# Performance work log

Hardware: AMD Instinct MI355X
Metric: run time of the kernel (lower is better)

Reference implementation:

```python
import jax, jax.numpy as jnp
import numpy as np

ALPHA = 3.0   # self.alpha
TAU = 0.1     # contrastive temperature
K = 8         # configs.k (top-k hyperedges per node)


def _scale(x, w, ehy, enod):
    """One scale of incidence_matrix_learn.
    x: [B, L, D] series tokens; w: [ws, D] word tokens;
    ehy: [H, D] hyperedge embedding table; enod: [N, D] node embedding table, N = L + ws.
    Returns (binary incidence matrix [N, H] float32, scalar contrastive loss).
    """
    B = x.shape[0]
    # concat_all[i]: cat(x.permute(0,2,1), word_expanded) -> [B, D, N]
    we = jnp.broadcast_to(w.T[None], (B,) + w.T.shape)          # [B, D, ws]
    concat = jnp.concatenate([jnp.transpose(x, (0, 2, 1)), we], axis=-1)  # [B, D, N]
    N, H = enod.shape[0], ehy.shape[0]
    # adjacency: softmax(relu(alpha * nodeec @ hyperen.T)) along hyperedge dim
    a = enod @ ehy.T                                            # [N, H]
    adj = jax.nn.softmax(jax.nn.relu(ALPHA * a), axis=-1)
    # top-k mask + threshold > 0.5 -> binary incidence matrix
    k = min(H, K)
    _, idx = jax.lax.top_k(adj, k)                              # [N, k]
    mask = jnp.zeros_like(adj).at[jnp.arange(N)[:, None], idx].set(1.0)
    adj_bin = ((adj * mask) > 0.5).astype(jnp.float32)          # [N, H]
    # positives: nodes sharing any hyperedge (build_pos_indices_from_edge_index),
    # equivalent to (A A^T > 0) with self excluded; dropping all-zero columns is a no-op here
    P = (adj_bin @ adj_bin.T > 0) & ~jnp.eye(N, dtype=bool)     # [N, N]
    cnt = P.sum(axis=1)                                         # positives per node
    # acl_loss_batched, vectorized over batch and nodes
    nodes = jnp.transpose(concat, (0, 2, 1))                    # [B, N, D]
    nrm = nodes / jnp.maximum(jnp.linalg.norm(nodes, axis=-1, keepdims=True), 1e-12)
    sim = jnp.einsum('bnd,bmd->bnm', nrm, nrm) / TAU            # [B, N, N]
    denom = jax.nn.logsumexp(sim, axis=-1)                      # [B, N]
    pos_mean = jnp.einsum('bnm,nm->bn', sim, P.astype(sim.dtype)) / jnp.maximum(cnt, 1)
    valid = cnt > 0                                             # [N]
    loss_sum = jnp.sum(jnp.where(valid[None, :], denom - pos_mean, 0.0))
    vc = B * valid.sum()
    loss = jnp.where(vc > 0, loss_sum / jnp.maximum(vc, 1), 0.0)
    return adj_bin, loss


def setup_inputs() -> dict:
    key = jax.random.key(0)
    ks = jax.random.split(key, 8)
    B, D = 64, 512
    return dict(
        x0=jax.random.normal(ks[0], (B, 512, D), dtype=jnp.float32),
        x1=jax.random.normal(ks[1], (B, 256, D), dtype=jnp.float32),
        word0=jax.random.normal(ks[2], (128, D), dtype=jnp.float32),
        word1=jax.random.normal(ks[3], (128, D), dtype=jnp.float32),
        embhy0=jax.random.normal(ks[4], (128, D), dtype=jnp.float32),
        embhy1=jax.random.normal(ks[5], (64, D), dtype=jnp.float32),
        embnod0=jax.random.normal(ks[6], (640, D), dtype=jnp.float32),
        embnod1=jax.random.normal(ks[7], (384, D), dtype=jnp.float32),
    )


def reference(x0, x1, word0, word1, embhy0, embhy1, embnod0, embnod1):
    a0, l0 = _scale(x0, word0, embhy0, embnod0)
    a1, l1 = _scale(x1, word1, embhy1, embnod1)
    return (a0, a1, l0 + l1)
```

## Files before the change

### kernel.cpp

```cpp
#include <hip/hip_runtime.h>


#define DDIM 512
#define BATCH 64
#define NGID 65536
#define NSLOT 5

typedef __attribute__((ext_vector_type(8))) short short8;
typedef __attribute__((ext_vector_type(4))) float f32x4;

__constant__ int PAIR_SCALE[21] = {0,0,0,0,0,0,0,0,0,0,0,0,0,0,0, 1,1,1,1,1,1};
__constant__ int PAIR_TU[21]    = {0,0,0,0,0,1,1,1,1,2,2,2,3,3,4, 0,0,0,1,1,2};
__constant__ int PAIR_TV[21]    = {0,1,2,3,4,1,2,3,4,2,3,4,3,4,4, 0,1,2,1,2,2};

__device__ __forceinline__ unsigned short f2bf(float f) {
  unsigned int u = __float_as_uint(f);
  u += 0x7fffu + ((u >> 16) & 1u);
  return (unsigned short)(u >> 16);
}

__device__ __forceinline__ void async16(const void* g, void* l) {
  __builtin_amdgcn_global_load_lds(
      (const __attribute__((address_space(1))) unsigned int*)g,
      (__attribute__((address_space(3))) unsigned int*)l, 16, 0, 0);
}

__global__ __launch_bounds__(256) void prep_kernel(
    const float* __restrict__ enod0, const float* __restrict__ ehy0,
    const float* __restrict__ enod1, const float* __restrict__ ehy1,
    float* __restrict__ adj0, float* __restrict__ adj1,
    int* __restrict__ labels0, int* __restrict__ labels1,
    const float* __restrict__ x0, const float* __restrict__ w0,
    const float* __restrict__ x1, const float* __restrict__ w1,
    unsigned short* __restrict__ nhat0, unsigned short* __restrict__ nhat1,
    float* __restrict__ acc, int* __restrict__ ticket) {
  const int t = threadIdx.x;
  if (blockIdx.x < 1024) {
    if (blockIdx.x == 0 && t == 0) { acc[0] = 0.f; acc[1] = 0.f; ticket[0] = 0; }
    const bool s0 = blockIdx.x < 640;
    const int n = s0 ? blockIdx.x : blockIdx.x - 640;
    const int H = s0 ? 128 : 64;
    const float* enod = s0 ? enod0 : enod1;
    const float* ehy = s0 ? ehy0 : ehy1;
    float* out_adj = s0 ? adj0 : adj1;
    int* labels = s0 ? labels0 : labels1;
    __shared__ float erow[DDIM];
    __shared__ float red[128];
    __shared__ int lab;
    if (t < 128) ((float4*)erow)[t] = ((const float4*)(enod + (size_t)n * DDIM))[t];
    if (t == 0) lab = -1;
    __syncthreads();
    float v = 0.f;
    if (t < H) {
      const float4* hr = (const float4*)(ehy + (size_t)t * DDIM);
      float a = 0.f;
      #pragma unroll 8
      for (int d = 0; d < DDIM / 4; ++d) {
        float4 h = hr[d];
        float4 e = ((const float4*)erow)[d];
        a = fmaf(h.x, e.x, a); a = fmaf(h.y, e.y, a);
        a = fmaf(h.z, e.z, a); a = fmaf(h.w, e.w, a);
      }
      v = fmaxf(0.f, 3.0f * a);
    }
    if (t < 128) red[t] = v;
    __syncthreads();
    for (int s = 64; s > 0; s >>= 1) {
      if (t < s) red[t] = fmaxf(red[t], red[t + s]);
      __syncthreads();
    }
    const float mx = red[0];
    __syncthreads();
    const float e = (t < H) ? __expf(v - mx) : 0.f;
    if (t < 128) red[t] = e;
    __syncthreads();
    for (int s = 64; s > 0; s >>= 1) {
      if (t < s) red[t] += red[t + s];
      __syncthreads();
    }
    const float sum = red[0];
    if (t < H) {
      const float adj = e / sum;
      const float bin = (adj > 0.5f) ? 1.0f : 0.0f;
      out_adj[(size_t)n * H + t] = bin;
      if (bin > 0.f) lab = t;
    }
    __syncthreads();
    if (t == 0) labels[n] = lab;
  } else {
    const int wave = t >> 6;
    const int lane = t & 63;
    const int g = (blockIdx.x - 1024) * 4 + wave;
    const bool s0 = g < BATCH * 640;
    const int gg = s0 ? g : g - BATCH * 640;
    const int N = s0 ? 640 : 384;
    const int L = s0 ? 512 : 256;
    const float* x = s0 ? x0 : x1;
    const float* w = s0 ? w0 : w1;
    unsigned short* nhat = s0 ? nhat0 : nhat1;
    const int b = gg / N;
    const int n = gg - b * N;
    const float* src = (n < L) ? (x + ((size_t)b * L + n) * DDIM)
                               : (w + (size_t)(n - L) * DDIM);
    const float4* rowp = (const float4*)src;
    const float4 v0 = rowp[lane];
    const float4 v1 = rowp[lane + 64];
    float ss = v0.x * v0.x + v0.y * v0.y + v0.z * v0.z + v0.w * v0.w +
               v1.x * v1.x + v1.y * v1.y + v1.z * v1.z + v1.w * v1.w;
    #pragma unroll
    for (int off = 32; off > 0; off >>= 1) ss += __shfl_xor(ss, off);
    const float rinv = 1.0f / fmaxf(sqrtf(ss), 1e-12f);
    ushort4 o0, o1;
    o0.x = f2bf(v0.x * rinv); o0.y = f2bf(v0.y * rinv);
    o0.z = f2bf(v0.z * rinv); o0.w = f2bf(v0.w * rinv);
    o1.x = f2bf(v1.x * rinv); o1.y = f2bf(v1.y * rinv);
    o1.z = f2bf(v1.z * rinv); o1.w = f2bf(v1.w * rinv);
    ushort4* op = (ushort4*)(nhat + ((size_t)b * N + n) * DDIM);
    op[lane] = o0;
    op[lane + 64] = o1;
  }
}

__global__ __launch_bounds__(256) void cnt_kernel(
    const int* __restrict__ labels0, int* __restrict__ cnt0,
    const int* __restrict__ labels1, int* __restrict__ cnt1,
    int* __restrict__ valid) {
  const bool s0 = blockIdx.x == 0;
  const int* labels = s0 ? labels0 : labels1;
  int* cnt = s0 ? cnt0 : cnt1;
  int* validcnt = s0 ? valid : valid + 1;
  const int N = s0 ? 640 : 384;
  __shared__ int lab[640];
  __shared__ int hist[128];
  __shared__ int vc;
  const int t = threadIdx.x;
  if (t == 0) vc = 0;
  if (t < 128) hist[t] = 0;
  for (int i = t; i < N; i += 256) lab[i] = labels[i];
  __syncthreads();
  for (int i = t; i < N; i += 256)
    if (lab[i] >= 0) atomicAdd(&hist[lab[i]], 1);
  __syncthreads();
  int lv = 0;
  for (int i = t; i < N; i += 256) {
    const int c = (lab[i] >= 0) ? hist[lab[i]] - 1 : 0;
    cnt[i] = c;
    if (c > 0) ++lv;
  }
  if (lv > 0) atomicAdd(&vc, lv);
  __syncthreads();
  if (t == 0) *validcnt = vc;
}

__global__ __launch_bounds__(256) void lse_kernel(
    const unsigned short* __restrict__ nhat0, const int* __restrict__ labels0,
    const unsigned short* __restrict__ nhat1, const int* __restrict__ labels1,
    float2* __restrict__ sp) {
  __shared__ short8 Abuf[2][1024];
  __shared__ short8 Bbuf[2][1024];
  __shared__ int labU[128], labV[128];
  __shared__ float2 rowBuf[128][2];
  __shared__ float2 colBuf[128][2];

  const int tid = threadIdx.x;
  const int p = blockIdx.x >> 6;
  const int b = blockIdx.x & 63;
  const bool s0 = PAIR_SCALE[p] == 0;
  const int tu = PAIR_TU[p], tv = PAIR_TV[p];
  const bool diag = (tu == tv);
  const int N = s0 ? 640 : 384;
  const unsigned short* nhat = s0 ? nhat0 : nhat1;
  const int* labels = s0 ? labels0 : labels1;
  const int gbase = s0 ? b * 640 : 40960 + b * 384;
  const size_t base = (size_t)b * N * DDIM;

  const int w = tid >> 6, lane = tid & 63;
  const int wr = w >> 1, wc = w & 1;
  const int lrow = lane & 15, lq = lane >> 4;

  if (tid < 128) labU[tid] = labels[tu * 128 + tid];
  else labV[tid - 128] = labels[tv * 128 + (tid - 128)];

  const unsigned short* Asrc = nhat + base + (size_t)tu * 128 * DDIM;
  const unsigned short* Bsrc = nhat + base + (size_t)tv * 128 * DDIM;

  #define STAGE(buf, kk)                                                     \
    do {                                                                     \
      _Pragma("unroll")                                                      \
      for (int i = 0; i < 4; ++i) {                                          \
        const int f = i * 4 + w;                                             \
        const int rg = f >> 1, ks = f & 1;                                   \
        const size_t so = (size_t)(rg * 16 + lrow) * DDIM +                  \
                          (kk) * 64 + ks * 32 + lq * 8;                      \
        async16(Asrc + so, &Abuf[buf][f * 64]);                              \
        async16(Bsrc + so, &Bbuf[buf][f * 64]);                              \
      }                                                                      \
    } while (0)

  f32x4 acc[4][4];
  #pragma unroll
  for (int mi = 0; mi < 4; ++mi)
    #pragma unroll
    for (int ni = 0; ni < 4; ++ni) acc[mi][ni] = (f32x4){0.f, 0.f, 0.f, 0.f};

  STAGE(0, 0);
  __syncthreads();

  for (int k = 0; k < 8; ++k) {
    const int cur = k & 1;
    if (k < 7) STAGE(cur ^ 1, k + 1);
    #pragma unroll
    for (int ks = 0; ks < 2; ++ks) {
      short8 am[4], bn[4];
      #pragma unroll
      for (int mi = 0; mi < 4; ++mi)
        am[mi] = Abuf[cur][((wr * 4 + mi) * 2 + ks) * 64 + lane];
      #pragma unroll
      for (int ni = 0; ni < 4; ++ni)
        bn[ni] = Bbuf[cur][((wc * 4 + ni) * 2 + ks) * 64 + lane];
      #pragma unroll
      for (int mi = 0; mi < 4; ++mi)
        #pragma unroll
        for (int ni = 0; ni < 4; ++ni)
          acc[mi][ni] = __builtin_amdgcn_mfma_f32_16x16x32_bf16(
              am[mi], bn[ni], acc[mi][ni], 0, 0, 0);
    }
    __syncthreads();
  }
  #undef STAGE

  float rSE[4][4], rPOS[4][4];
  float cSE[4] = {0.f, 0.f, 0.f, 0.f};
  float cPOS[4] = {0.f, 0.f, 0.f, 0.f};
  int labn[4][4], labm[4];
  #pragma unroll
  for (int mi = 0; mi < 4; ++mi)
    #pragma unroll
    for (int r = 0; r < 4; ++r) {
      rSE[mi][r] = 0.f; rPOS[mi][r] = 0.f;
      labn[mi][r] = labU[wr * 64 + mi * 16 + lq * 4 + r];
    }
  #pragma unroll
  for (int ni = 0; ni < 4; ++ni) labm[ni] = labV[wc * 64 + ni * 16 + lrow];

  #pragma unroll
  for (int mi = 0; mi < 4; ++mi) {
    const int u_loc = wr * 64 + mi * 16 + lq * 4;
    #pragma unroll
    for (int ni = 0; ni < 4; ++ni) {
      const int v_loc = wc * 64 + ni * 16 + lrow;
      #pragma unroll
      for (int r = 0; r < 4; ++r) {
        const float sim = acc[mi][ni][r] * 10.0f;
        const float e = __expf(sim - 10.0f);
        rSE[mi][r] += e;
        const bool match = (labn[mi][r] >= 0) && (labm[ni] == labn[mi][r]);
        const bool self = diag && (u_loc + r == v_loc);
        if (match && !self) rPOS[mi][r] += sim;
        if (!diag) {
          cSE[ni] += e;
          if (match) cPOS[ni] += sim;
        }
      }
    }
  }

  #pragma unroll
  for (int off = 1; off <= 8; off <<= 1)
    #pragma unroll
    for (int mi = 0; mi < 4; ++mi)
      #pragma unroll
      for (int r = 0; r < 4; ++r) {
        rSE[mi][r] += __shfl_xor(rSE[mi][r], off);
        rPOS[mi][r] += __shfl_xor(rPOS[mi][r], off);
      }
  if (lrow == 0) {
    #pragma unroll
    for (int mi = 0; mi < 4; ++mi)
      #pragma unroll
      for (int r = 0; r < 4; ++r) {
        float2 st; st.x = rSE[mi][r]; st.y = rPOS[mi][r];
        rowBuf[wr * 64 + mi * 16 + lq * 4 + r][wc] = st;
      }
  }
  if (!diag) {
    #pragma unroll
    for (int off = 16; off <= 32; off <<= 1)
      #pragma unroll
      for (int ni = 0; ni < 4; ++ni) {
        cSE[ni] += __shfl_xor(cSE[ni], off);
        cPOS[ni] += __shfl_xor(cPOS[ni], off);
      }
    if (lane < 16) {
      #pragma unroll
      for (int ni = 0; ni < 4; ++ni) {
        float2 st; st.x = cSE[ni]; st.y = cPOS[ni];
        colBuf[wc * 64 + ni * 16 + lrow][wr] = st;
      }
    }
  }
  __syncthreads();
  if (tid < 128) {
    const float2 ra = rowBuf[tid][0], rb = rowBuf[tid][1];
    float2 st; st.x = ra.x + rb.x; st.y = ra.y + rb.y;
    sp[(size_t)tv * NGID + gbase + tu * 128 + tid] = st;
    if (!diag) {
      const float2 ca = colBuf[tid][0], cb = colBuf[tid][1];
      float2 ct; ct.x = ca.x + cb.x; ct.y = ca.y + cb.y;
      sp[(size_t)tu * NGID + gbase + tv * 128 + tid] = ct;
    }
  }
}

__global__ __launch_bounds__(256) void loss_reduce(
    const float2* __restrict__ sp, const int* __restrict__ cnt0,
    const int* __restrict__ cnt1, float* __restrict__ acc,
    const int* __restrict__ valid, int* __restrict__ ticket,
    float* __restrict__ lossp) {
  __shared__ float r0[4], r1[4];
  const int t = threadIdx.x;
  float l0 = 0.f, l1 = 0.f;
  for (int g = blockIdx.x * 256 + t; g < NGID; g += 64 * 256) {
    const bool is0 = g < 40960;
    const int n = is0 ? (g % 640) : ((g - 40960) % 384);
    const int nslots = is0 ? 5 : 3;
    float se = 0.f, pos = 0.f;
    for (int s = 0; s < nslots; ++s) {
      const float2 v = sp[(size_t)s * NGID + g];
      se += v.x; pos += v.y;
    }
    const int c = is0 ? cnt0[n] : cnt1[n];
    if (c > 0) {
      const float v = (10.0f + logf(se)) - pos / (float)c;
      if (is0) l0 += v; else l1 += v;
    }
  }
  #pragma unroll
  for (int off = 32; off > 0; off >>= 1) {
    l0 += __shfl_xor(l0, off);
    l1 += __shfl_xor(l1, off);
  }
  if ((t & 63) == 0) { r0[t >> 6] = l0; r1[t >> 6] = l1; }
  __syncthreads();
  if (t == 0) {
    atomicAdd(&acc[0], r0[0] + r0[1] + r0[2] + r0[3]);
    atomicAdd(&acc[1], r1[0] + r1[1] + r1[2] + r1[3]);
    __threadfence();
    const int done = atomicAdd(ticket, 1);
    if (done == 63) {
      const float a0v = atomicAdd(&acc[0], 0.0f);
      const float a1v = atomicAdd(&acc[1], 0.0f);
      float l = 0.f;
      if (valid[0] > 0) l += a0v / (float)(BATCH * valid[0]);
      if (valid[1] > 0) l += a1v / (float)(BATCH * valid[1]);
      lossp[0] = l;
    }
  }
}

extern "C" void kernel_launch(void* const* d_in, const int* in_sizes, int n_in,
                              void* d_out, int out_size, void* d_ws,
                              size_t ws_size, hipStream_t stream) {
  const float* x0 = (const float*)d_in[0];
  const float* x1 = (const float*)d_in[1];
  const float* w0 = (const float*)d_in[2];
  const float* w1 = (const float*)d_in[3];
  const float* ehy0 = (const float*)d_in[4];
  const float* ehy1 = (const float*)d_in[5];
  const float* enod0 = (const float*)d_in[6];
  const float* enod1 = (const float*)d_in[7];

  float* out = (float*)d_out;
  float* adj0 = out;
  float* adj1 = out + 640 * 128;
  float* lossp = out + 640 * 128 + 384 * 64;

  unsigned short* nhat0 = (unsigned short*)d_ws;
  unsigned short* nhat1 = nhat0 + (size_t)BATCH * 640 * DDIM;
  int* ip = (int*)(nhat1 + (size_t)BATCH * 384 * DDIM);
  int* labels0 = ip;
  int* labels1 = labels0 + 640;
  int* cnt0 = labels1 + 384;
  int* cnt1 = cnt0 + 640;
  int* valid = cnt1 + 384;
  int* ticket = valid + 2;
  float* acc = (float*)(ticket + 1);
  float2* sp = (float2*)((((size_t)(acc + 2)) + 255) & ~(size_t)255);

  prep_kernel<<<1024 + 16384, 256, 0, stream>>>(
      enod0, ehy0, enod1, ehy1, adj0, adj1, labels0, labels1,
      x0, w0, x1, w1, nhat0, nhat1, acc, ticket);
  cnt_kernel<<<2, 256, 0, stream>>>(labels0, cnt0, labels1, cnt1, valid);
  lse_kernel<<<1344, 256, 0, stream>>>(nhat0, labels0, nhat1, labels1, sp);
  loss_reduce<<<64, 256, 0, stream>>>(sp, cnt0, cnt1, acc, valid, ticket,
                                      lossp);
}
```

Before: 235.0 us.

## Triple-buffer lse_kernel K loop and fold count kernel into loss reduction

The lse_kernel main loop moves from a double-buffered 64-wide K step with full __syncthreads to a 32-wide step with three LDS slots. It uses explicit vmcnt waits and a raw s_barrier, which keeps two async loads in flight while the MFMAs run. The separate cnt_kernel launch is removed, and every loss_reduce block now recomputes the label histograms and valid counts in shared memory. This saves one kernel launch and the dependency between kernels, at the cost of repeating the histogram work in all 64 reduce blocks and running more barriers per K in the GEMM.

```diff
diff --git a/kernel.cpp b/kernel.cpp
--- a/kernel.cpp
+++ b/kernel.cpp
@@ -4,7 +4,6 @@
 #define DDIM 512
 #define BATCH 64
 #define NGID 65536
-#define NSLOT 5
 
 typedef __attribute__((ext_vector_type(8))) short short8;
 typedef __attribute__((ext_vector_type(4))) float f32x4;
@@ -121,43 +120,12 @@
   }
 }
 
-__global__ __launch_bounds__(256) void cnt_kernel(
-    const int* __restrict__ labels0, int* __restrict__ cnt0,
-    const int* __restrict__ labels1, int* __restrict__ cnt1,
-    int* __restrict__ valid) {
-  const bool s0 = blockIdx.x == 0;
-  const int* labels = s0 ? labels0 : labels1;
-  int* cnt = s0 ? cnt0 : cnt1;
-  int* validcnt = s0 ? valid : valid + 1;
-  const int N = s0 ? 640 : 384;
-  __shared__ int lab[640];
-  __shared__ int hist[128];
-  __shared__ int vc;
-  const int t = threadIdx.x;
-  if (t == 0) vc = 0;
-  if (t < 128) hist[t] = 0;
-  for (int i = t; i < N; i += 256) lab[i] = labels[i];
-  __syncthreads();
-  for (int i = t; i < N; i += 256)
-    if (lab[i] >= 0) atomicAdd(&hist[lab[i]], 1);
-  __syncthreads();
-  int lv = 0;
-  for (int i = t; i < N; i += 256) {
-    const int c = (lab[i] >= 0) ? hist[lab[i]] - 1 : 0;
-    cnt[i] = c;
-    if (c > 0) ++lv;
-  }
-  if (lv > 0) atomicAdd(&vc, lv);
-  __syncthreads();
-  if (t == 0) *validcnt = vc;
-}
-
 __global__ __launch_bounds__(256) void lse_kernel(
     const unsigned short* __restrict__ nhat0, const int* __restrict__ labels0,
     const unsigned short* __restrict__ nhat1, const int* __restrict__ labels1,
     float2* __restrict__ sp) {
-  __shared__ short8 Abuf[2][1024];
-  __shared__ short8 Bbuf[2][1024];
+  __shared__ short8 Abuf[3][512];
+  __shared__ short8 Bbuf[3][512];
   __shared__ int labU[128], labV[128];
   __shared__ float2 rowBuf[128][2];
   __shared__ float2 colBuf[128][2];
@@ -184,16 +152,14 @@
   const unsigned short* Asrc = nhat + base + (size_t)tu * 128 * DDIM;
   const unsigned short* Bsrc = nhat + base + (size_t)tv * 128 * DDIM;
 
-  #define STAGE(buf, kk)                                                     \
+  #define STAGE(slot, cc)                                                    \
     do {                                                                     \
       _Pragma("unroll")                                                      \
-      for (int i = 0; i < 4; ++i) {                                          \
-        const int f = i * 4 + w;                                             \
-        const int rg = f >> 1, ks = f & 1;                                   \
-        const size_t so = (size_t)(rg * 16 + lrow) * DDIM +                  \
-                          (kk) * 64 + ks * 32 + lq * 8;                      \
-        async16(Asrc + so, &Abuf[buf][f * 64]);                              \
-        async16(Bsrc + so, &Bbuf[buf][f * 64]);                              \
+      for (int i = 0; i < 2; ++i) {                                          \
+        const int f = w * 2 + i;                                             \
+        const size_t so = (size_t)(f * 16 + lrow) * DDIM + (cc) * 32 + lq * 8;\
+        async16(Asrc + so, &Abuf[slot][f * 64]);                             \
+        async16(Bsrc + so, &Bbuf[slot][f * 64]);                             \
       }                                                                      \
     } while (0)
 
@@ -204,28 +170,27 @@
     for (int ni = 0; ni < 4; ++ni) acc[mi][ni] = (f32x4){0.f, 0.f, 0.f, 0.f};
 
   STAGE(0, 0);
-  __syncthreads();
-
-  for (int k = 0; k < 8; ++k) {
-    const int cur = k & 1;
-    if (k < 7) STAGE(cur ^ 1, k + 1);
-    #pragma unroll
-    for (int ks = 0; ks < 2; ++ks) {
-      short8 am[4], bn[4];
-      #pragma unroll
-      for (int mi = 0; mi < 4; ++mi)
-        am[mi] = Abuf[cur][((wr * 4 + mi) * 2 + ks) * 64 + lane];
+  STAGE(1, 1);
+
+  #pragma unroll
+  for (int c = 0; c < 16; ++c) {
+    if (c < 15) asm volatile("s_waitcnt vmcnt(4)" ::: "memory");
+    else        asm volatile("s_waitcnt vmcnt(0)" ::: "memory");
+    __builtin_amdgcn_s_barrier();
+    if (c < 14) STAGE((c + 2) % 3, c + 2);
+    const short8* Ab = &Abuf[c % 3][0];
+    const short8* Bb = &Bbuf[c % 3][0];
+    short8 am[4], bn[4];
+    #pragma unroll
+    for (int mi = 0; mi < 4; ++mi) am[mi] = Ab[(wr * 4 + mi) * 64 + lane];
+    #pragma unroll
+    for (int ni = 0; ni < 4; ++ni) bn[ni] = Bb[(wc * 4 + ni) * 64 + lane];
+    #pragma unroll
+    for (int mi = 0; mi < 4; ++mi)
       #pragma unroll
       for (int ni = 0; ni < 4; ++ni)
-        bn[ni] = Bbuf[cur][((wc * 4 + ni) * 2 + ks) * 64 + lane];
-      #pragma unroll
-      for (int mi = 0; mi < 4; ++mi)
-        #pragma unroll
-        for (int ni = 0; ni < 4; ++ni)
-          acc[mi][ni] = __builtin_amdgcn_mfma_f32_16x16x32_bf16(
-              am[mi], bn[ni], acc[mi][ni], 0, 0, 0);
-    }
-    __syncthreads();
+        acc[mi][ni] = __builtin_amdgcn_mfma_f32_16x16x32_bf16(
+            am[mi], bn[ni], acc[mi][ni], 0, 0, 0);
   }
   #undef STAGE
 
@@ -313,12 +278,34 @@
 }
 
 __global__ __launch_bounds__(256) void loss_reduce(
-    const float2* __restrict__ sp, const int* __restrict__ cnt0,
-    const int* __restrict__ cnt1, float* __restrict__ acc,
-    const int* __restrict__ valid, int* __restrict__ ticket,
-    float* __restrict__ lossp) {
+    const float2* __restrict__ sp, const int* __restrict__ labels0,
+    const int* __restrict__ labels1, float* __restrict__ acc,
+    int* __restrict__ ticket, float* __restrict__ lossp) {
+  __shared__ int lab0[640], lab1[384];
+  __shared__ int hist0[128], hist1[64];
+  __shared__ int vcS[2];
   __shared__ float r0[4], r1[4];
   const int t = threadIdx.x;
+  if (t < 128) hist0[t] = 0;
+  else if (t < 192) hist1[t - 128] = 0;
+  if (t < 2) vcS[t] = 0;
+  for (int i = t; i < 640; i += 256) lab0[i] = labels0[i];
+  for (int i = t; i < 384; i += 256) lab1[i] = labels1[i];
+  __syncthreads();
+  for (int i = t; i < 640; i += 256)
+    if (lab0[i] >= 0) atomicAdd(&hist0[lab0[i]], 1);
+  for (int i = t; i < 384; i += 256)
+    if (lab1[i] >= 0) atomicAdd(&hist1[lab1[i]], 1);
+  __syncthreads();
+  int lv0 = 0, lv1 = 0;
+  for (int i = t; i < 640; i += 256)
+    if (lab0[i] >= 0 && hist0[lab0[i]] >= 2) ++lv0;
+  for (int i = t; i < 384; i += 256)
+    if (lab1[i] >= 0 && hist1[lab1[i]] >= 2) ++lv1;
+  if (lv0 > 0) atomicAdd(&vcS[0], lv0);
+  if (lv1 > 0) atomicAdd(&vcS[1], lv1);
+  __syncthreads();
+
   float l0 = 0.f, l1 = 0.f;
   for (int g = blockIdx.x * 256 + t; g < NGID; g += 64 * 256) {
     const bool is0 = g < 40960;
@@ -329,7 +316,8 @@
       const float2 v = sp[(size_t)s * NGID + g];
       se += v.x; pos += v.y;
     }
-    const int c = is0 ? cnt0[n] : cnt1[n];
+    const int lb = is0 ? lab0[n] : lab1[n];
+    const int c = (lb >= 0) ? ((is0 ? hist0[lb] : hist1[lb]) - 1) : 0;
     if (c > 0) {
       const float v = (10.0f + logf(se)) - pos / (float)c;
       if (is0) l0 += v; else l1 += v;
@@ -351,8 +339,8 @@
       const float a0v = atomicAdd(&acc[0], 0.0f);
       const float a1v = atomicAdd(&acc[1], 0.0f);
       float l = 0.f;
-      if (valid[0] > 0) l += a0v / (float)(BATCH * valid[0]);
-      if (valid[1] > 0) l += a1v / (float)(BATCH * valid[1]);
+      if (vcS[0] > 0) l += a0v / (float)(BATCH * vcS[0]);
+      if (vcS[1] > 0) l += a1v / (float)(BATCH * vcS[1]);
       lossp[0] = l;
     }
   }
@@ -380,18 +368,14 @@
   int* ip = (int*)(nhat1 + (size_t)BATCH * 384 * DDIM);
   int* labels0 = ip;
   int* labels1 = labels0 + 640;
-  int* cnt0 = labels1 + 384;
-  int* cnt1 = cnt0 + 640;
-  int* valid = cnt1 + 384;
-  int* ticket = valid + 2;
+  int* ticket = labels1 + 384;
   float* acc = (float*)(ticket + 1);
   float2* sp = (float2*)((((size_t)(acc + 2)) + 255) & ~(size_t)255);
 
   prep_kernel<<<1024 + 16384, 256, 0, stream>>>(
       enod0, ehy0, enod1, ehy1, adj0, adj1, labels0, labels1,
       x0, w0, x1, w1, nhat0, nhat1, acc, ticket);
-  cnt_kernel<<<2, 256, 0, stream>>>(labels0, cnt0, labels1, cnt1, valid);
   lse_kernel<<<1344, 256, 0, stream>>>(nhat0, labels0, nhat1, labels1, sp);
-  loss_reduce<<<64, 256, 0, stream>>>(sp, cnt0, cnt1, acc, valid, ticket,
+  loss_reduce<<<64, 256, 0, stream>>>(sp, labels0, labels1, acc, ticket,
                                       lossp);
 }
```

New measurement: 237.7 us. Within noise of the previous version (+1.2%).
